# Performance work log

Measured on AMD Instinct MI355X. Metric: run time of the kernel, lower is better.

The kernel has to match this reference:

```python
import jax, jax.numpy as jnp
import numpy as np

E, K = 8, 2          # num_experts, top_k
D, I = 1024, 2048    # hidden_dim, intermediate_dim
B, S = 4, 1024       # batch, seq_len


def setup_inputs() -> dict:
    key = jax.random.key(0)
    k0, k1, k2, k3, k4 = jax.random.split(key, 5)
    hidden_states = jax.random.normal(k0, (B, S, D), dtype=jnp.float32)
    Wc = jax.random.normal(k1, (E, D), dtype=jnp.float32) * (1.0 / np.sqrt(D))
    bc = jnp.zeros((E,), dtype=jnp.float32)
    Wg = jax.random.normal(k2, (E, D, I), dtype=jnp.float32) * (1.0 / np.sqrt(D))
    Wu = jax.random.normal(k3, (E, D, I), dtype=jnp.float32) * (1.0 / np.sqrt(D))
    Wd = jax.random.normal(k4, (E, I, D), dtype=jnp.float32) * (1.0 / np.sqrt(I))
    return {"hidden_states": hidden_states, "Wc": Wc, "bc": bc,
            "Wg": Wg, "Wu": Wu, "Wd": Wd}


def reference(hidden_states, Wc, bc, Wg, Wu, Wd):
    b, s, d = hidden_states.shape
    x = hidden_states.reshape(-1, d)                       # [T, D]
    # Confidence heads: one scalar per (token, expert), sigmoid-activated.
    conf = jax.nn.sigmoid(jnp.einsum('td,ed->te', x, Wc) + bc)  # [T, E]
    # Auction routing: top_k by confidence, softmax over selected bids.
    top_vals, top_idx = jax.lax.top_k(conf, K)             # [T, K]
    rweights = jax.nn.softmax(top_vals, axis=-1)           # [T, K]
    # Combine weights per (token, expert): sum_k rw_k * one_hot(idx_k).
    comb = jnp.sum(jax.nn.one_hot(top_idx, E, dtype=x.dtype)
                   * rweights[..., None], axis=1)          # [T, E]
    # SwiGLU experts (dense compute over all experts, sparse combine).
    g = jnp.einsum('td,edi->tei', x, Wg)                   # [T, E, I]
    u = jnp.einsum('td,edi->tei', x, Wu)                   # [T, E, I]
    h = jax.nn.silu(g) * u                                 # [T, E, I]
    y = jnp.einsum('tei,eid->ted', h, Wd)                  # [T, E, D]
    out = jnp.einsum('ted,te->td', y, comb)                # [T, D]
    return out.reshape(b, s, d)
```

## Files before the change

kernel.cpp:

```cpp
#include <hip/hip_runtime.h>

#define T_TOK 4096
#define DDIM  1024
#define IDIM  2048
#define NE    8
#define TOTROWS 8192

typedef unsigned short u16;
typedef unsigned int   u32;
typedef _Float16 f16;
typedef _Float16 f16x8 __attribute__((ext_vector_type(8)));
typedef _Float16 f16x4 __attribute__((ext_vector_type(4)));
typedef float    f32x16 __attribute__((ext_vector_type(16)));

static __device__ __forceinline__ void gload16(const f16* g, f16* l) {
  __builtin_amdgcn_global_load_lds(
      (const __attribute__((address_space(1))) void*)g,
      (__attribute__((address_space(3))) void*)l, 16, 0, 0);
}

__global__ __launch_bounds__(256) void conf_kernel(
    const float* __restrict__ x, const float* __restrict__ Wc,
    const float* __restrict__ bc, float* __restrict__ conf)
{
  int gid  = blockIdx.x * 256 + threadIdx.x;
  int t    = gid >> 6;
  int lane = threadIdx.x & 63;
  if (t >= T_TOK) return;
  const float* xr = x + (size_t)t * DDIM;
  float acc[NE];
#pragma unroll
  for (int e = 0; e < NE; e++) acc[e] = 0.f;
  for (int d = lane; d < DDIM; d += 64) {
    float xv = xr[d];
#pragma unroll
    for (int e = 0; e < NE; e++) acc[e] += xv * Wc[e * DDIM + d];
  }
#pragma unroll
  for (int off = 32; off > 0; off >>= 1) {
#pragma unroll
    for (int e = 0; e < NE; e++) acc[e] += __shfl_down(acc[e], off, 64);
  }
  if (lane == 0) {
#pragma unroll
    for (int e = 0; e < NE; e++)
      conf[t * NE + e] = 1.f / (1.f + expf(-(acc[e] + bc[e])));
  }
}

__global__ __launch_bounds__(256) void top2_kernel(
    const float* __restrict__ conf,
    int* __restrict__ counts, int* __restrict__ list, float* __restrict__ wlist)
{
  int t = blockIdx.x * 256 + threadIdx.x;
  if (t >= T_TOK) return;
  float c[NE];
#pragma unroll
  for (int e = 0; e < NE; e++) c[e] = conf[t * NE + e];
  int i0 = 0;
#pragma unroll
  for (int e = 1; e < NE; e++) if (c[e] > c[i0]) i0 = e;
  int i1 = (i0 == 0) ? 1 : 0;
#pragma unroll
  for (int e = 0; e < NE; e++) if (e != i0 && c[e] > c[i1]) i1 = e;
  float w1 = 1.f / (1.f + expf(c[i0] - c[i1]));
  float w0 = 1.f - w1;
  int s0 = atomicAdd(&counts[i0], 1);
  list[i0 * T_TOK + s0]  = t;
  wlist[i0 * T_TOK + s0] = w0;
  int s1 = atomicAdd(&counts[i1], 1);
  list[i1 * T_TOK + s1]  = t;
  wlist[i1 * T_TOK + s1] = w1;
}

__global__ void scan_kernel(const int* __restrict__ counts, int* __restrict__ base)
{
  if (threadIdx.x == 0 && blockIdx.x == 0) {
    int s = 0;
    for (int e = 0; e < NE; e++) { base[e] = s; s += counts[e]; }
    base[NE] = s;
  }
}

__global__ __launch_bounds__(256) void cvt_x_kernel(
    const float* __restrict__ x, f16* __restrict__ xh)
{
  int i = blockIdx.x * 256 + threadIdx.x;
  float4 v = ((const float4*)x)[i];
  f16x4 h; h[0] = (f16)v.x; h[1] = (f16)v.y; h[2] = (f16)v.z; h[3] = (f16)v.w;
  ((f16x4*)xh)[i] = h;
}

__global__ __launch_bounds__(256) void tpose_kernel(
    const float* __restrict__ in, f16* __restrict__ out, int R, int C)
{
  __shared__ float t[32][33];
  const size_t mat = (size_t)R * C;
  const float* src = in  + (size_t)blockIdx.z * mat;
  f16*         dst = out + (size_t)blockIdx.z * mat;
  int c0 = blockIdx.x * 32, r0 = blockIdx.y * 32;
  int tx = threadIdx.x & 31, ty = threadIdx.x >> 5;
#pragma unroll
  for (int i = 0; i < 32; i += 8)
    t[ty + i][tx] = src[(size_t)(r0 + ty + i) * C + c0 + tx];
  __syncthreads();
#pragma unroll
  for (int i = 0; i < 32; i += 8)
    dst[(size_t)(c0 + ty + i) * R + r0 + tx] = (f16)t[tx][ty + i];
}

constexpr int BM = 128, BN = 128, BK = 64;

__global__ __launch_bounds__(256, 2) void gemm1_kernel(
    const f16* __restrict__ xh, const f16* __restrict__ WgT, const f16* __restrict__ WuT,
    const int* __restrict__ counts, const int* __restrict__ base,
    const int* __restrict__ list, const float* __restrict__ wlist,
    f16* __restrict__ hbuf)
{
  const int e   = blockIdx.z;
  const int cnt = counts[e];
  const int p0  = blockIdx.y * BM;
  if (p0 >= cnt) return;
  const int n0  = blockIdx.x * BN;

  __shared__ __align__(16) f16 As [BM * BK];
  __shared__ __align__(16) f16 Bgs[BN * BK];
  __shared__ __align__(16) f16 Bus[BN * BK];
  __shared__ int   tokS[BM];
  __shared__ float wS[BM];

  const int tid = threadIdx.x;
  if (tid < BM) {
    int p = p0 + tid;
    tokS[tid] = (p < cnt) ? list[e * T_TOK + p] : 0;
    wS[tid]   = (p < cnt) ? wlist[e * T_TOK + p] : 0.f;
  }
  __syncthreads();

  const int l  = tid & 63;
  const int w  = tid >> 6;
  const int wr = w >> 1, wc = w & 1;
  const int rl = l >> 3;
  const int sl = (l & 7) ^ rl;
  const int lm = l & 31;
  const int kg = l >> 5;

  const f16* ga[4]; const f16* gg[4]; const f16* gu[4];
  const f16* WgE = WgT + ((size_t)e << 21);
  const f16* WuE = WuT + ((size_t)e << 21);
#pragma unroll
  for (int ii = 0; ii < 4; ii++) {
    int i = w * 4 + ii;
    int r = i * 8 + rl;
    ga[ii] = xh  + (size_t)tokS[r] * DDIM + sl * 8;
    gg[ii] = WgE + (size_t)(n0 + r) * DDIM + sl * 8;
    gu[ii] = WuE + (size_t)(n0 + r) * DDIM + sl * 8;
  }

  f32x16 accg[2][2], accu[2][2];
#pragma unroll
  for (int a = 0; a < 2; a++)
#pragma unroll
    for (int b = 0; b < 2; b++)
#pragma unroll
      for (int r = 0; r < 16; r++) { accg[a][b][r] = 0.f; accu[a][b][r] = 0.f; }

  for (int kt = 0; kt < DDIM / BK; kt++) {
    const int k0 = kt * BK;
#pragma unroll
    for (int ii = 0; ii < 4; ii++) {
      int i = w * 4 + ii;
      gload16(ga[ii] + k0, &As [i * 512]);
      gload16(gg[ii] + k0, &Bgs[i * 512]);
      gload16(gu[ii] + k0, &Bus[i * 512]);
    }
    __syncthreads();
#pragma unroll
    for (int ks = 0; ks < 4; ks++) {
      f16x8 av[2], bg[2], bu[2];
#pragma unroll
      for (int mr = 0; mr < 2; mr++) {
        int R = wr * 64 + mr * 32 + lm;
        int slot = (ks * 2 + kg) ^ (R & 7);
        av[mr] = *(const f16x8*)&As[R * 64 + slot * 8];
      }
#pragma unroll
      for (int nc = 0; nc < 2; nc++) {
        int R = wc * 64 + nc * 32 + lm;
        int slot = (ks * 2 + kg) ^ (R & 7);
        bg[nc] = *(const f16x8*)&Bgs[R * 64 + slot * 8];
        bu[nc] = *(const f16x8*)&Bus[R * 64 + slot * 8];
      }
#pragma unroll
      for (int mr = 0; mr < 2; mr++)
#pragma unroll
        for (int nc = 0; nc < 2; nc++) {
          accg[mr][nc] = __builtin_amdgcn_mfma_f32_32x32x16_f16(av[mr], bg[nc], accg[mr][nc], 0, 0, 0);
          accu[mr][nc] = __builtin_amdgcn_mfma_f32_32x32x16_f16(av[mr], bu[nc], accu[mr][nc], 0, 0, 0);
        }
    }
    __syncthreads();
  }

  const int rowbase = base[e] + p0;
  const int rbase4  = kg * 4;
#pragma unroll
  for (int mr = 0; mr < 2; mr++)
#pragma unroll
    for (int nc = 0; nc < 2; nc++) {
      int ncol = n0 + wc * 64 + nc * 32 + lm;
#pragma unroll
      for (int r = 0; r < 16; r++) {
        int rin = (r & 3) + ((r >> 2) << 3) + rbase4;
        int p   = wr * 64 + mr * 32 + rin;
        if (p0 + p < cnt) {
          float g = accg[mr][nc][r], u = accu[mr][nc][r];
          float h = g / (1.f + expf(-g)) * u * wS[p];
          hbuf[(size_t)(rowbase + p) * IDIM + ncol] = (f16)h;
        }
      }
    }
}

__global__ __launch_bounds__(256, 2) void gemm2_kernel(
    const f16* __restrict__ hbuf, const f16* __restrict__ WdT,
    const int* __restrict__ counts, const int* __restrict__ base,
    const int* __restrict__ list, float* __restrict__ out)
{
  const int e   = blockIdx.z;
  const int cnt = counts[e];
  const int p0  = blockIdx.y * BM;
  if (p0 >= cnt) return;
  const int n0  = blockIdx.x * BN;

  __shared__ __align__(16) f16 Hs [BM * BK];
  __shared__ __align__(16) f16 Bds[BN * BK];
  __shared__ int tokS[BM];

  const int tid = threadIdx.x;
  if (tid < BM) {
    int p = p0 + tid;
    tokS[tid] = (p < cnt) ? list[e * T_TOK + p] : 0;
  }
  __syncthreads();

  const int l  = tid & 63;
  const int w  = tid >> 6;
  const int wr = w >> 1, wc = w & 1;
  const int rl = l >> 3;
  const int sl = (l & 7) ^ rl;
  const int lm = l & 31;
  const int kg = l >> 5;

  const int rowbase = base[e] + p0;
  const f16* WdE = WdT + ((size_t)e << 21);

  const f16* ga[4]; const f16* gd[4];
#pragma unroll
  for (int ii = 0; ii < 4; ii++) {
    int i = w * 4 + ii;
    int r = i * 8 + rl;
    int hr = rowbase + r; if (hr > TOTROWS - 1) hr = TOTROWS - 1;
    ga[ii] = hbuf + (size_t)hr * IDIM + sl * 8;
    gd[ii] = WdE  + (size_t)(n0 + r) * IDIM + sl * 8;
  }

  f32x16 acc[2][2];
#pragma unroll
  for (int a = 0; a < 2; a++)
#pragma unroll
    for (int b = 0; b < 2; b++)
#pragma unroll
      for (int r = 0; r < 16; r++) acc[a][b][r] = 0.f;

  for (int kt = 0; kt < IDIM / BK; kt++) {
    const int k0 = kt * BK;
#pragma unroll
    for (int ii = 0; ii < 4; ii++) {
      int i = w * 4 + ii;
      gload16(ga[ii] + k0, &Hs [i * 512]);
      gload16(gd[ii] + k0, &Bds[i * 512]);
    }
    __syncthreads();
#pragma unroll
    for (int ks = 0; ks < 4; ks++) {
      f16x8 av[2], bd[2];
#pragma unroll
      for (int mr = 0; mr < 2; mr++) {
        int R = wr * 64 + mr * 32 + lm;
        int slot = (ks * 2 + kg) ^ (R & 7);
        av[mr] = *(const f16x8*)&Hs[R * 64 + slot * 8];
      }
#pragma unroll
      for (int nc = 0; nc < 2; nc++) {
        int R = wc * 64 + nc * 32 + lm;
        int slot = (ks * 2 + kg) ^ (R & 7);
        bd[nc] = *(const f16x8*)&Bds[R * 64 + slot * 8];
      }
#pragma unroll
      for (int mr = 0; mr < 2; mr++)
#pragma unroll
        for (int nc = 0; nc < 2; nc++)
          acc[mr][nc] = __builtin_amdgcn_mfma_f32_32x32x16_f16(av[mr], bd[nc], acc[mr][nc], 0, 0, 0);
    }
    __syncthreads();
  }

  const int rbase4 = kg * 4;
#pragma unroll
  for (int mr = 0; mr < 2; mr++)
#pragma unroll
    for (int nc = 0; nc < 2; nc++) {
      int ncol = n0 + wc * 64 + nc * 32 + lm;
#pragma unroll
      for (int r = 0; r < 16; r++) {
        int rin = (r & 3) + ((r >> 2) << 3) + rbase4;
        int p   = wr * 64 + mr * 32 + rin;
        if (p0 + p < cnt)
          atomicAdd(&out[(size_t)tokS[p] * DDIM + ncol], acc[mr][nc][r]);
      }
    }
}

extern "C" void kernel_launch(void* const* d_in, const int* in_sizes, int n_in,
                              void* d_out, int out_size, void* d_ws, size_t ws_size,
                              hipStream_t stream)
{
  const float* x  = (const float*)d_in[0];
  const float* Wc = (const float*)d_in[1];
  const float* bc = (const float*)d_in[2];
  const float* Wg = (const float*)d_in[3];
  const float* Wu = (const float*)d_in[4];
  const float* Wd = (const float*)d_in[5];
  float* out = (float*)d_out;

  char* ws = (char*)d_ws;
  int*   counts = (int*)(ws + 0);
  int*   base   = (int*)(ws + 256);
  float* conf   = (float*)(ws + 1024);
  int*   list   = (int*)(ws + 132096);
  float* wlist  = (float*)(ws + 263168);
  f16*   xh     = (f16*)(ws + 394240);
  f16*   hbuf   = (f16*)(ws + 8782848);
  f16*   W1     = (f16*)(ws + 42337280);
  f16*   W2     = (f16*)(ws + 75891712);

  hipMemsetAsync(counts, 0, 64, stream);
  hipMemsetAsync(out, 0, (size_t)out_size * sizeof(float), stream);

  conf_kernel<<<T_TOK / 4, 256, 0, stream>>>(x, Wc, bc, conf);
  top2_kernel<<<T_TOK / 256, 256, 0, stream>>>(conf, counts, list, wlist);
  scan_kernel<<<1, 64, 0, stream>>>(counts, base);

  cvt_x_kernel<<<T_TOK * DDIM / 1024, 256, 0, stream>>>(x, xh);
  dim3 gt1(IDIM / 32, DDIM / 32, NE);
  tpose_kernel<<<gt1, 256, 0, stream>>>(Wg, W1, DDIM, IDIM);
  tpose_kernel<<<gt1, 256, 0, stream>>>(Wu, W2, DDIM, IDIM);

  dim3 g1(IDIM / BN, T_TOK / BM, NE);
  gemm1_kernel<<<g1, 256, 0, stream>>>(xh, W1, W2, counts, base, list, wlist, hbuf);

  dim3 gt2(DDIM / 32, IDIM / 32, NE);
  tpose_kernel<<<gt2, 256, 0, stream>>>(Wd, W1, IDIM, DDIM);

  dim3 g2(DDIM / BN, T_TOK / BM, NE);
  gemm2_kernel<<<g2, 256, 0, stream>>>(hbuf, W1, counts, base, list, out);
}
```

Before: 463.1 us.

## Double-buffer LDS tiles and switch GEMMs to 16x16x32 MFMA with BK=32

Both expert GEMM kernels now use two LDS buffers with BK=32. The next k-tile is loaded asynchronously while MFMAs run on the current one, and each iteration needs one barrier instead of two. The MFMA shape changes from 32x32x16 to 16x16x32 with 4x4 fragments per wave, and the LDS swizzle is reworked for the narrower tile. The aim is to overlap global-to-LDS loads with compute. The cost is twice as many k-iterations, and the smaller MFMA may have lower per-instruction throughput.

```diff
diff --git a/kernel.cpp b/kernel.cpp
--- a/kernel.cpp
+++ b/kernel.cpp
@@ -11,7 +11,7 @@
 typedef _Float16 f16;
 typedef _Float16 f16x8 __attribute__((ext_vector_type(8)));
 typedef _Float16 f16x4 __attribute__((ext_vector_type(4)));
-typedef float    f32x16 __attribute__((ext_vector_type(16)));
+typedef float    f32x4 __attribute__((ext_vector_type(4)));
 
 static __device__ __forceinline__ void gload16(const f16* g, f16* l) {
   __builtin_amdgcn_global_load_lds(
@@ -109,7 +109,7 @@
     dst[(size_t)(c0 + ty + i) * R + r0 + tx] = (f16)t[tx][ty + i];
 }
 
-constexpr int BM = 128, BN = 128, BK = 64;
+constexpr int BK = 32;
 
 __global__ __launch_bounds__(256, 2) void gemm1_kernel(
     const f16* __restrict__ xh, const f16* __restrict__ WgT, const f16* __restrict__ WuT,
@@ -119,104 +119,104 @@
 {
   const int e   = blockIdx.z;
   const int cnt = counts[e];
-  const int p0  = blockIdx.y * BM;
+  const int p0  = blockIdx.y * 128;
   if (p0 >= cnt) return;
-  const int n0  = blockIdx.x * BN;
-
-  __shared__ __align__(16) f16 As [BM * BK];
-  __shared__ __align__(16) f16 Bgs[BN * BK];
-  __shared__ __align__(16) f16 Bus[BN * BK];
-  __shared__ int   tokS[BM];
-  __shared__ float wS[BM];
+  const int n0  = blockIdx.x * 128;
+
+  __shared__ __align__(16) f16 As [2][128 * BK];
+  __shared__ __align__(16) f16 Bgs[2][128 * BK];
+  __shared__ __align__(16) f16 Bus[2][128 * BK];
+  __shared__ int   tokS[128];
+  __shared__ float wS[128];
 
   const int tid = threadIdx.x;
-  if (tid < BM) {
+  if (tid < 128) {
     int p = p0 + tid;
     tokS[tid] = (p < cnt) ? list[e * T_TOK + p] : 0;
     wS[tid]   = (p < cnt) ? wlist[e * T_TOK + p] : 0.f;
   }
   __syncthreads();
 
-  const int l  = tid & 63;
-  const int w  = tid >> 6;
-  const int wr = w >> 1, wc = w & 1;
-  const int rl = l >> 3;
-  const int sl = (l & 7) ^ rl;
-  const int lm = l & 31;
-  const int kg = l >> 5;
-
-  const f16* ga[4]; const f16* gg[4]; const f16* gu[4];
+  const int l   = tid & 63;
+  const int w   = tid >> 6;
+  const int wr  = w >> 1, wc = w & 1;
+  const int r15 = l & 15;
+  const int kg  = l >> 4;
+
+  const int rl4 = l >> 2;
+  const int sl  = (l & 3) ^ ((l >> 3) & 3);
   const f16* WgE = WgT + ((size_t)e << 21);
   const f16* WuE = WuT + ((size_t)e << 21);
-#pragma unroll
-  for (int ii = 0; ii < 4; ii++) {
-    int i = w * 4 + ii;
-    int r = i * 8 + rl;
-    ga[ii] = xh  + (size_t)tokS[r] * DDIM + sl * 8;
-    gg[ii] = WgE + (size_t)(n0 + r) * DDIM + sl * 8;
-    gu[ii] = WuE + (size_t)(n0 + r) * DDIM + sl * 8;
-  }
-
-  f32x16 accg[2][2], accu[2][2];
-#pragma unroll
-  for (int a = 0; a < 2; a++)
-#pragma unroll
-    for (int b = 0; b < 2; b++)
-#pragma unroll
-      for (int r = 0; r < 16; r++) { accg[a][b][r] = 0.f; accu[a][b][r] = 0.f; }
-
-  for (int kt = 0; kt < DDIM / BK; kt++) {
-    const int k0 = kt * BK;
-#pragma unroll
-    for (int ii = 0; ii < 4; ii++) {
-      int i = w * 4 + ii;
-      gload16(ga[ii] + k0, &As [i * 512]);
-      gload16(gg[ii] + k0, &Bgs[i * 512]);
-      gload16(gu[ii] + k0, &Bus[i * 512]);
+  const f16* srcA[2]; const f16* srcG[2]; const f16* srcU[2];
+#pragma unroll
+  for (int ii = 0; ii < 2; ii++) {
+    int j = 2 * w + ii;
+    int row = j * 16 + rl4;
+    srcA[ii] = xh  + (size_t)tokS[row] * DDIM + sl * 8;
+    srcG[ii] = WgE + (size_t)(n0 + row) * DDIM + sl * 8;
+    srcU[ii] = WuE + (size_t)(n0 + row) * DDIM + sl * 8;
+  }
+
+  const int phys = kg ^ ((r15 >> 1) & 3);
+  const int aoff = (wr * 64 + r15) * BK + phys * 8;
+  const int boff = (wc * 64 + r15) * BK + phys * 8;
+
+  f32x4 accg[4][4], accu[4][4];
+#pragma unroll
+  for (int a = 0; a < 4; a++)
+#pragma unroll
+    for (int bq = 0; bq < 4; bq++)
+#pragma unroll
+      for (int r = 0; r < 4; r++) { accg[a][bq][r] = 0.f; accu[a][bq][r] = 0.f; }
+
+#define STAGE1(KT, B) do {                                   \
+    int koff = (KT) * BK;                                    \
+    _Pragma("unroll")                                        \
+    for (int ii = 0; ii < 2; ii++) {                         \
+      int j = 2 * w + ii;                                    \
+      gload16(srcA[ii] + koff, &As [B][j * 512]);            \
+      gload16(srcG[ii] + koff, &Bgs[B][j * 512]);            \
+      gload16(srcU[ii] + koff, &Bus[B][j * 512]);            \
+    }                                                        \
+  } while (0)
+
+  STAGE1(0, 0);
+  constexpr int NT = DDIM / BK;
+  for (int kt = 0; kt < NT; kt++) {
+    const int b = kt & 1;
+    __syncthreads();
+    if (kt + 1 < NT) STAGE1(kt + 1, b ^ 1);
+
+    f16x8 av[4], bgv[4], buv[4];
+#pragma unroll
+    for (int mi = 0; mi < 4; mi++) av[mi] = *(const f16x8*)&As[b][aoff + mi * 512];
+#pragma unroll
+    for (int ni = 0; ni < 4; ni++) {
+      bgv[ni] = *(const f16x8*)&Bgs[b][boff + ni * 512];
+      buv[ni] = *(const f16x8*)&Bus[b][boff + ni * 512];
     }
-    __syncthreads();
-#pragma unroll
-    for (int ks = 0; ks < 4; ks++) {
-      f16x8 av[2], bg[2], bu[2];
-#pragma unroll
-      for (int mr = 0; mr < 2; mr++) {
-        int R = wr * 64 + mr * 32 + lm;
-        int slot = (ks * 2 + kg) ^ (R & 7);
-        av[mr] = *(const f16x8*)&As[R * 64 + slot * 8];
+#pragma unroll
+    for (int mi = 0; mi < 4; mi++)
+#pragma unroll
+      for (int ni = 0; ni < 4; ni++) {
+        accg[mi][ni] = __builtin_amdgcn_mfma_f32_16x16x32_f16(av[mi], bgv[ni], accg[mi][ni], 0, 0, 0);
+        accu[mi][ni] = __builtin_amdgcn_mfma_f32_16x16x32_f16(av[mi], buv[ni], accu[mi][ni], 0, 0, 0);
       }
-#pragma unroll
-      for (int nc = 0; nc < 2; nc++) {
-        int R = wc * 64 + nc * 32 + lm;
-        int slot = (ks * 2 + kg) ^ (R & 7);
-        bg[nc] = *(const f16x8*)&Bgs[R * 64 + slot * 8];
-        bu[nc] = *(const f16x8*)&Bus[R * 64 + slot * 8];
-      }
-#pragma unroll
-      for (int mr = 0; mr < 2; mr++)
-#pragma unroll
-        for (int nc = 0; nc < 2; nc++) {
-          accg[mr][nc] = __builtin_amdgcn_mfma_f32_32x32x16_f16(av[mr], bg[nc], accg[mr][nc], 0, 0, 0);
-          accu[mr][nc] = __builtin_amdgcn_mfma_f32_32x32x16_f16(av[mr], bu[nc], accu[mr][nc], 0, 0, 0);
-        }
-    }
-    __syncthreads();
-  }
+  }
+#undef STAGE1
 
   const int rowbase = base[e] + p0;
-  const int rbase4  = kg * 4;
-#pragma unroll
-  for (int mr = 0; mr < 2; mr++)
-#pragma unroll
-    for (int nc = 0; nc < 2; nc++) {
-      int ncol = n0 + wc * 64 + nc * 32 + lm;
-#pragma unroll
-      for (int r = 0; r < 16; r++) {
-        int rin = (r & 3) + ((r >> 2) << 3) + rbase4;
-        int p   = wr * 64 + mr * 32 + rin;
+#pragma unroll
+  for (int mi = 0; mi < 4; mi++)
+#pragma unroll
+    for (int ni = 0; ni < 4; ni++) {
+      int col = n0 + wc * 64 + ni * 16 + r15;
+#pragma unroll
+      for (int r = 0; r < 4; r++) {
+        int p = wr * 64 + mi * 16 + kg * 4 + r;
         if (p0 + p < cnt) {
-          float g = accg[mr][nc][r], u = accu[mr][nc][r];
-          float h = g / (1.f + expf(-g)) * u * wS[p];
-          hbuf[(size_t)(rowbase + p) * IDIM + ncol] = (f16)h;
+          float g = accg[mi][ni][r], u = accu[mi][ni][r];
+          hbuf[(size_t)(rowbase + p) * IDIM + col] = (f16)(g / (1.f + expf(-g)) * u * wS[p]);
         }
       }
     }
@@ -229,95 +229,93 @@
 {
   const int e   = blockIdx.z;
   const int cnt = counts[e];
-  const int p0  = blockIdx.y * BM;
+  const int p0  = blockIdx.y * 128;
   if (p0 >= cnt) return;
-  const int n0  = blockIdx.x * BN;
-
-  __shared__ __align__(16) f16 Hs [BM * BK];
-  __shared__ __align__(16) f16 Bds[BN * BK];
-  __shared__ int tokS[BM];
+  const int n0  = blockIdx.x * 128;
+
+  __shared__ __align__(16) f16 Hs [2][128 * BK];
+  __shared__ __align__(16) f16 Bds[2][128 * BK];
+  __shared__ int tokS[128];
 
   const int tid = threadIdx.x;
-  if (tid < BM) {
+  if (tid < 128) {
     int p = p0 + tid;
     tokS[tid] = (p < cnt) ? list[e * T_TOK + p] : 0;
   }
   __syncthreads();
 
-  const int l  = tid & 63;
-  const int w  = tid >> 6;
-  const int wr = w >> 1, wc = w & 1;
-  const int rl = l >> 3;
-  const int sl = (l & 7) ^ rl;
-  const int lm = l & 31;
-  const int kg = l >> 5;
-
+  const int l   = tid & 63;
+  const int w   = tid >> 6;
+  const int wr  = w >> 1, wc = w & 1;
+  const int r15 = l & 15;
+  const int kg  = l >> 4;
+
+  const int rl4 = l >> 2;
+  const int sl  = (l & 3) ^ ((l >> 3) & 3);
   const int rowbase = base[e] + p0;
   const f16* WdE = WdT + ((size_t)e << 21);
-
-  const f16* ga[4]; const f16* gd[4];
-#pragma unroll
-  for (int ii = 0; ii < 4; ii++) {
-    int i = w * 4 + ii;
-    int r = i * 8 + rl;
-    int hr = rowbase + r; if (hr > TOTROWS - 1) hr = TOTROWS - 1;
-    ga[ii] = hbuf + (size_t)hr * IDIM + sl * 8;
-    gd[ii] = WdE  + (size_t)(n0 + r) * IDIM + sl * 8;
-  }
-
-  f32x16 acc[2][2];
-#pragma unroll
-  for (int a = 0; a < 2; a++)
-#pragma unroll
-    for (int b = 0; b < 2; b++)
-#pragma unroll
-      for (int r = 0; r < 16; r++) acc[a][b][r] = 0.f;
-
-  for (int kt = 0; kt < IDIM / BK; kt++) {
-    const int k0 = kt * BK;
-#pragma unroll
-    for (int ii = 0; ii < 4; ii++) {
-      int i = w * 4 + ii;
-      gload16(ga[ii] + k0, &Hs [i * 512]);
-      gload16(gd[ii] + k0, &Bds[i * 512]);
-    }
+  const f16* srcH[2]; const f16* srcD[2];
+#pragma unroll
+  for (int ii = 0; ii < 2; ii++) {
+    int j = 2 * w + ii;
+    int row = j * 16 + rl4;
+    int hr = rowbase + row; if (hr > TOTROWS - 1) hr = TOTROWS - 1;
+    srcH[ii] = hbuf + (size_t)hr * IDIM + sl * 8;
+    srcD[ii] = WdE  + (size_t)(n0 + row) * IDIM + sl * 8;
+  }
+
+  const int phys = kg ^ ((r15 >> 1) & 3);
+  const int aoff = (wr * 64 + r15) * BK + phys * 8;
+  const int boff = (wc * 64 + r15) * BK + phys * 8;
+
+  f32x4 acc[4][4];
+#pragma unroll
+  for (int a = 0; a < 4; a++)
+#pragma unroll
+    for (int bq = 0; bq < 4; bq++)
+#pragma unroll
+      for (int r = 0; r < 4; r++) acc[a][bq][r] = 0.f;
+
+#define STAGE2(KT, B) do {                                   \
+    int koff = (KT) * BK;                                    \
+    _Pragma("unroll")                                        \
+    for (int ii = 0; ii < 2; ii++) {                         \
+      int j = 2 * w + ii;                                    \
+      gload16(srcH[ii] + koff, &Hs [B][j * 512]);            \
+      gload16(srcD[ii] + koff, &Bds[B][j * 512]);            \
+    }                                                        \
+  } while (0)
+
+  STAGE2(0, 0);
+  constexpr int NT = IDIM / BK;
+  for (int kt = 0; kt < NT; kt++) {
+    const int b = kt & 1;
     __syncthreads();
-#pragma unroll
-    for (int ks = 0; ks < 4; ks++) {
-      f16x8 av[2], bd[2];
-#pragma unroll
-      for (int mr = 0; mr < 2; mr++) {
-        int R = wr * 64 + mr * 32 + lm;
-        int slot = (ks * 2 + kg) ^ (R & 7);
-        av[mr] = *(const f16x8*)&Hs[R * 64 + slot * 8];
-      }
-#pragma unroll
-      for (int nc = 0; nc < 2; nc++) {
-        int R = wc * 64 + nc * 32 + lm;
-        int slot = (ks * 2 + kg) ^ (R & 7);
-        bd[nc] = *(const f16x8*)&Bds[R * 64 + slot * 8];
-      }
-#pragma unroll
-      for (int mr = 0; mr < 2; mr++)
-#pragma unroll
-        for (int nc = 0; nc < 2; nc++)
-          acc[mr][nc] = __builtin_amdgcn_mfma_f32_32x32x16_f16(av[mr], bd[nc], acc[mr][nc], 0, 0, 0);
-    }
-    __syncthreads();
-  }
-
-  const int rbase4 = kg * 4;
-#pragma unroll
-  for (int mr = 0; mr < 2; mr++)
-#pragma unroll
-    for (int nc = 0; nc < 2; nc++) {
-      int ncol = n0 + wc * 64 + nc * 32 + lm;
-#pragma unroll
-      for (int r = 0; r < 16; r++) {
-        int rin = (r & 3) + ((r >> 2) << 3) + rbase4;
-        int p   = wr * 64 + mr * 32 + rin;
+    if (kt + 1 < NT) STAGE2(kt + 1, b ^ 1);
+
+    f16x8 av[4], bdv[4];
+#pragma unroll
+    for (int mi = 0; mi < 4; mi++) av[mi] = *(const f16x8*)&Hs[b][aoff + mi * 512];
+#pragma unroll
+    for (int ni = 0; ni < 4; ni++) bdv[ni] = *(const f16x8*)&Bds[b][boff + ni * 512];
+#pragma unroll
+    for (int mi = 0; mi < 4; mi++)
+#pragma unroll
+      for (int ni = 0; ni < 4; ni++)
+        acc[mi][ni] = __builtin_amdgcn_mfma_f32_16x16x32_f16(av[mi], bdv[ni], acc[mi][ni], 0, 0, 0);
+  }
+#undef STAGE2
+
+#pragma unroll
+  for (int mi = 0; mi < 4; mi++)
+#pragma unroll
+    for (int ni = 0; ni < 4; ni++) {
+      int col = n0 + wc * 64 + ni * 16 + r15;
+#pragma unroll
+      for (int r = 0; r < 4; r++) {
+        int p = wr * 64 + mi * 16 + kg * 4 + r;
         if (p0 + p < cnt)
-          atomicAdd(&out[(size_t)tokS[p] * DDIM + ncol], acc[mr][nc][r]);
+          atomicAdd(&out[(size_t)tokS[p] * DDIM + col], acc[mi][ni][r]);
       }
     }
 }
@@ -357,12 +355,12 @@
   tpose_kernel<<<gt1, 256, 0, stream>>>(Wg, W1, DDIM, IDIM);
   tpose_kernel<<<gt1, 256, 0, stream>>>(Wu, W2, DDIM, IDIM);
 
-  dim3 g1(IDIM / BN, T_TOK / BM, NE);
+  dim3 g1(IDIM / 128, T_TOK / 128, NE);
   gemm1_kernel<<<g1, 256, 0, stream>>>(xh, W1, W2, counts, base, list, wlist, hbuf);
 
   dim3 gt2(DDIM / 32, IDIM / 32, NE);
   tpose_kernel<<<gt2, 256, 0, stream>>>(Wd, W1, IDIM, DDIM);
 
-  dim3 g2(DDIM / BN, T_TOK / BM, NE);
+  dim3 g2(DDIM / 128, T_TOK / 128, NE);
   gemm2_kernel<<<g2, 256, 0, stream>>>(hbuf, W1, counts, base, list, out);
 }
```

Result: slower. 499.4 us (+7.9%).
